# Kernel optimization log

Measured on AMD Instinct MI355X. Metric: run time of the kernel, lower is better.

The kernel has to match this reference:

```python
import jax, jax.numpy as jnp
import numpy as np

N, C_IN, C_OUT, T, V, K = 32, 64, 128, 300, 25, 3
EPS = 1e-5


def setup_inputs() -> dict:
    key = jax.random.key(0)
    ks = jax.random.split(key, 10)
    x = jax.random.normal(ks[0], (N, C_IN, T, V), dtype=jnp.float32)
    # fixed adjacency buffer (requires_grad=False in torch) and learned attention mask
    A = jax.random.uniform(ks[1], (K, V, V), dtype=jnp.float32)
    graph_attn = jnp.ones((K, V, V), dtype=jnp.float32)  # nn.init.constant_(1)
    # per-subset 1x1 conv weights/biases, stacked: [K, C_out, C_in]
    Wg = jax.random.normal(ks[2], (K, C_OUT, C_IN), dtype=jnp.float32) * np.sqrt(2.0 / (C_OUT * K))
    bg = jnp.zeros((K, C_OUT), dtype=jnp.float32)
    # main BN affine (torch init: weight=1e-6, bias=0; use small random for a nontrivial test)
    bn_gamma = jax.random.normal(ks[3], (C_OUT,), dtype=jnp.float32) * 0.1 + 1.0
    bn_beta = jax.random.normal(ks[4], (C_OUT,), dtype=jnp.float32) * 0.1
    # residual branch (in != out): 1x1 conv + BN
    Wr = jax.random.normal(ks[5], (C_OUT, C_IN), dtype=jnp.float32) * np.sqrt(2.0 / C_IN)
    br = jnp.zeros((C_OUT,), dtype=jnp.float32)
    rbn_gamma = jax.random.normal(ks[6], (C_OUT,), dtype=jnp.float32) * 0.1 + 1.0
    rbn_beta = jax.random.normal(ks[7], (C_OUT,), dtype=jnp.float32) * 0.1
    return {"x": x, "A": A, "graph_attn": graph_attn, "Wg": Wg, "bg": bg,
            "bn_gamma": bn_gamma, "bn_beta": bn_beta,
            "Wr": Wr, "br": br, "rbn_gamma": rbn_gamma, "rbn_beta": rbn_beta}


def _batchnorm(z, gamma, beta):
    # training-mode BatchNorm2d: biased batch stats over (N, T, V)
    mean = jnp.mean(z, axis=(0, 2, 3), keepdims=True)
    var = jnp.var(z, axis=(0, 2, 3), keepdims=True)
    zhat = (z - mean) * jax.lax.rsqrt(var + EPS)
    return zhat * gamma[None, :, None, None] + beta[None, :, None, None]


def reference(x, A, graph_attn, Wg, bg, bn_gamma, bn_beta, Wr, br, rbn_gamma, rbn_beta):
    Ae = A * graph_attn                                   # [K, V, V]
    # per-subset graph aggregation: (x.view(N, C*T, V) @ Ae[k])  -> [K, N, C, T, V]
    xA = jnp.einsum('nctv,kvw->knctw', x, Ae)
    # per-subset 1x1 conv then sum over subsets; biases sum as well
    hidden = jnp.einsum('knctv,koc->notv', xA, Wg) + jnp.sum(bg, axis=0)[None, :, None, None]
    hidden = _batchnorm(hidden, bn_gamma, bn_beta)
    # residual: 1x1 conv + BN (since in_channels != out_channels)
    res = jnp.einsum('nctv,oc->notv', x, Wr) + br[None, :, None, None]
    res = _batchnorm(res, rbn_gamma, rbn_beta)
    return hidden + res
```

## Files before the change

### kernel.cpp

```cpp
#include <hip/hip_runtime.h>

typedef __attribute__((ext_vector_type(8))) _Float16 half8;
typedef __attribute__((ext_vector_type(4))) _Float16 half4v;
typedef __attribute__((ext_vector_type(4))) float float4v;
typedef float float4u __attribute__((ext_vector_type(4), aligned(4)));
typedef unsigned long long u64;
typedef unsigned int u32;

#define NB   32
#define CIN  64
#define COUT 128
#define TT   300
#define VV   25
#define EPS  1e-5f
#define M_TOT 240000.0f
#define NBLK 1600
#define NTILE 4800

#define WS_WF    0
#define WS_AEF   65536
#define WS_ST    73728
#define WS_CF    75776
#define WS_WF2   77312
#define WS_HR    1048576
#define WS_PARTP (WS_HR + 137625600)
#define WS_NEED  (WS_PARTP + 3276800)

__device__ __forceinline__ void bar_lds() {
    __builtin_amdgcn_sched_barrier(0);
    asm volatile("s_waitcnt lgkmcnt(0)" ::: "memory");
    __builtin_amdgcn_s_barrier();
    __builtin_amdgcn_sched_barrier(0);
}

__device__ __forceinline__ unsigned short f2h(float f) {
    return __builtin_bit_cast(unsigned short, (_Float16)f);
}
__device__ __forceinline__ float4v mfma16(half8 a, half8 b, float4v c) {
    return __builtin_amdgcn_mfma_f32_16x16x32_f16(a, b, c, 0, 0, 0);
}
__device__ __forceinline__ u32 pk2(float a, float b) {
    return __builtin_bit_cast(u32, __builtin_amdgcn_cvt_pkrtz(a, b));
}
__device__ __forceinline__ int hr_off(int cm, int on) {
    return (cm & 1) ? (2048 + (cm >> 1) * 768 + on * 384)
                    : ((cm >> 1) * 1024 + on * 512);
}

__global__ void prep_kernel(const float* __restrict__ A, const float* __restrict__ ga,
                            const float* __restrict__ Wg, const float* __restrict__ Wr,
                            char* __restrict__ wsb) {
    unsigned short* wf = (unsigned short*)(wsb + WS_WF);
    unsigned short* ae = (unsigned short*)(wsb + WS_AEF);
    float* st = (float*)(wsb + WS_ST);
    int i = blockIdx.x * blockDim.x + threadIdx.x;
    for (; i < 32768 + 4096 + 512; i += gridDim.x * blockDim.x) {
        if (i < 32768) {
            int on = i >> 12, kt = (i >> 9) & 7, l = (i >> 3) & 63, j = i & 7;
            int o = on * 16 + (l & 15);
            int kc = kt * 32 + ((l >> 4) << 3) + j;
            float v = (kc < 192) ? Wg[((kc >> 6) * COUT + o) * CIN + (kc & 63)]
                                 : Wr[o * CIN + (kc - 192)];
            wf[i] = f2h(v);
        } else if (i < 32768 + 4096) {
            int q = i - 32768;
            int k = q >> 10, nt = (q >> 9) & 1, l = (q >> 3) & 63, j = q & 7;
            int v = ((l >> 4) << 3) + j, w = nt * 16 + (l & 15);
            float val = 0.0f;
            if (v < VV && w < VV)
                val = (k < 3) ? A[(k * VV + v) * VV + w] * ga[(k * VV + v) * VV + w]
                              : (v == w ? 1.0f : 0.0f);
            ae[q] = f2h(val);
        } else {
            st[i - 36864] = 0.0f;
        }
    }
}

__global__ __launch_bounds__(256) void red_kernel(const float* __restrict__ part,
                                                  char* __restrict__ wsb) {
    float* st = (float*)(wsb + WS_ST);
    __shared__ float red[4][4];
    const int tid = threadIdx.x, wv = tid >> 6, lane = tid & 63;
    const int i0 = blockIdx.x * 4;
    const int bi = tid >> 2, ii = tid & 3;
    float s = 0.0f;
    for (int b = bi; b < NBLK; b += 64)
        s += part[(size_t)b * 512 + i0 + ii];
    s += __shfl_xor(s, 4);
    s += __shfl_xor(s, 8);
    s += __shfl_xor(s, 16);
    s += __shfl_xor(s, 32);
    if (lane < 4) red[wv][lane] = s;
    __syncthreads();
    if (tid < 4) st[i0 + tid] = red[0][tid] + red[1][tid] + red[2][tid] + red[3][tid];
}

__global__ __launch_bounds__(256) void scale_kernel(
        const float* __restrict__ Wg, const float* __restrict__ Wr,
        const float* __restrict__ g1, const float* __restrict__ b1,
        const float* __restrict__ g2, const float* __restrict__ b2,
        char* __restrict__ wsb, int fillw2) {
    const float* st = (const float*)(wsb + WS_ST);
    float* cf = (float*)(wsb + WS_CF);
    unsigned short* wf2 = (unsigned short*)(wsb + WS_WF2);
    __shared__ float cl[384];
    int tid = threadIdx.x;
    if (tid < 128) {
        int o = tid;
        const float inv_m = 1.0f / M_TOT;
        float mH = st[o] * inv_m,        vH = st[128 + o] * inv_m - mH * mH;
        float mR = st[256 + o] * inv_m,  vR = st[384 + o] * inv_m - mR * mR;
        float scH = g1[o] * rsqrtf(vH + EPS);
        float scR = g2[o] * rsqrtf(vR + EPS);
        float bC  = b1[o] + b2[o] - scH * mH - scR * mR;
        cl[o] = scH; cl[128 + o] = scR; cl[256 + o] = bC;
        if (blockIdx.x == 0) { cf[o] = scH; cf[128 + o] = scR; cf[256 + o] = bC; }
    }
    __syncthreads();
    if (!fillw2) return;
    for (int i = blockIdx.x * 256 + tid; i < 32768; i += gridDim.x * 256) {
        int on = i >> 12, kt = (i >> 9) & 7, l = (i >> 3) & 63, j = i & 7;
        int o = on * 16 + (l & 15);
        int kc = kt * 32 + ((l >> 4) << 3) + j;
        float v = (kc < 192) ? Wg[((kc >> 6) * COUT + o) * CIN + (kc & 63)] * cl[o]
                             : Wr[o * CIN + (kc - 192)] * cl[128 + o];
        wf2[i] = f2h(v);
    }
}

template <int MODE>
__global__ __launch_bounds__(256, 2) void gcn_kernel(
        const float* __restrict__ x, char* __restrict__ wsb, float* __restrict__ out,
        float* __restrict__ part) {
    __shared__ __align__(16) _Float16 xa[64 * 256];
    __shared__ __align__(16) _Float16 xs[2][64][32];
    char* xab = (char*)xa;

    const unsigned short* wf = (const unsigned short*)(wsb + (MODE == 1 ? WS_WF2 : WS_WF));
    const unsigned short* ae = (const unsigned short*)(wsb + WS_AEF);
    const float* cf = (const float*)(wsb + WS_CF);

    const int tid = threadIdx.x, wv = tid >> 6, l = tid & 63;
    const int l15 = l & 15, lq = l >> 4;

    half8 af[2][8];
#pragma unroll
    for (int on = 0; on < 2; ++on)
#pragma unroll
        for (int kt = 0; kt < 8; ++kt)
            af[on][kt] = *(const half8*)&wf[(((wv * 2 + on) * 8 + kt) * 64 + l) * 8];

    half8 aef[4][2];
#pragma unroll
    for (int k = 0; k < 4; ++k)
#pragma unroll
        for (int nt = 0; nt < 2; ++nt)
            aef[k][nt] = *(const half8*)&ae[((k * 2 + nt) * 64 + l) * 8];

    float bC2[2];
    if (MODE == 1) {
#pragma unroll
        for (int on = 0; on < 2; ++on)
            bC2[on] = cf[256 + wv * 32 + on * 16 + l15];
    }

    float sH[2], sH2[2], sR[2], sR2[2];
    if (MODE != 1) {
#pragma unroll
        for (int on = 0; on < 2; ++on) { sH[on] = 0; sH2[on] = 0; sR[on] = 0; sR2[on] = 0; }
    }

    for (int e = tid; e < 896; e += 256) {
        int t = e / 448, r = e % 448;
        xs[t][r / 7][25 + r % 7] = (_Float16)0.0f;
    }

    float4v pre[4];
    auto issue_pre = [&](int n_, int t0_) {
#pragma unroll
        for (int p = 0; p < 4; ++p) {
            int idx = tid + p * 256;
            int c = idx >> 4, i = idx & 15;
            int f0 = i * 4; f0 = f0 > 46 ? 46 : f0;
            const float* g = x + n_ * 480000 + c * 7500 + t0_ * 25 + f0;
            float4u v = *(const float4u*)g;
            pre[p][0] = v[0]; pre[p][1] = v[1]; pre[p][2] = v[2]; pre[p][3] = v[3];
        }
    };
    auto write_xs = [&]() {
#pragma unroll
        for (int p = 0; p < 4; ++p) {
            int idx = tid + p * 256;
            int c = idx >> 4, i = idx & 15;
            int f0 = i * 4; f0 = f0 > 46 ? 46 : f0;
#pragma unroll
            for (int s = 0; s < 4; ++s) {
                int f = f0 + s;
                int tsel = (f >= 25) ? 1 : 0;
                xs[tsel][c][f - tsel * 25] = (_Float16)pre[p][s];
            }
        }
    };

    const int tile0 = blockIdx.x * 3;
    { int n0 = tile0 / 150, t00 = (tile0 % 150) * 2; issue_pre(n0, t00); }
    write_xs();

    for (int it = 0; it < 3; ++it) {
        const int tile = tile0 + it;
        const int n = tile / 150, t0 = (tile % 150) * 2;
        bar_lds();

        const bool hn = (it < 2);
        if (hn) { int tl = tile + 1; issue_pre(tl / 150, (tl % 150) * 2); }

#pragma unroll
        for (int t = 0; t < 2; ++t) {
            half8 xf = *(const half8*)&xs[t][wv * 16 + l15][lq * 8];
#pragma unroll
            for (int k = 0; k < 4; ++k)
#pragma unroll
                for (int nt = 0; nt < 2; ++nt) {
                    float4v c4 = {0.0f, 0.0f, 0.0f, 0.0f};
                    c4 = mfma16(xf, aef[k][nt], c4);
                    int col = t * 32 + nt * 16 + l15;
                    int kcb = (k * 64 + wv * 16 + lq * 4) * 2;
                    u64 pk = ((u64)pk2(c4[2], c4[3]) << 32) | pk2(c4[0], c4[1]);
                    *(u64*)(xab + ((col << 9) + (kcb ^ ((col & 7) << 4)))) = pk;
                }
        }
        bar_lds();

        char* hrw = wsb + WS_HR + (size_t)tile * 28672 + wv * 7168;

        float4v acc[4][2];
        if (MODE != 1) {
#pragma unroll
            for (int cm = 0; cm < 4; ++cm)
#pragma unroll
                for (int on = 0; on < 2; ++on) acc[cm][on] = {0.0f, 0.0f, 0.0f, 0.0f};
#pragma unroll
            for (int kt = 0; kt < 6; ++kt)
#pragma unroll
                for (int cm = 0; cm < 4; ++cm) {
                    int col = cm * 16 + l15;
                    half8 bf = *(const half8*)(xab + ((col << 9) +
                                   ((kt * 64 + lq * 16) ^ ((col & 7) << 4))));
                    acc[cm][0] = mfma16(bf, af[0][kt], acc[cm][0]);
                    acc[cm][1] = mfma16(bf, af[1][kt], acc[cm][1]);
                }
#pragma unroll
            for (int cm = 0; cm < 4; ++cm)
#pragma unroll
                for (int on = 0; on < 2; ++on) {
#pragma unroll
                    for (int r = 0; r < 4; ++r) {
                        float h = acc[cm][on][r];
                        sH[on] += h; sH2[on] += h * h;
                    }
                    if (MODE == 2) {
                        u64 p = (u64)pk2(acc[cm][on][0], acc[cm][on][1]) |
                                ((u64)pk2(acc[cm][on][2], acc[cm][on][3]) << 32);
                        if (!(cm & 1)) {
                            *(u64*)(hrw + hr_off(cm, on) + l * 8) = p;
                        } else if (lq < 3) {
                            *(u64*)(hrw + hr_off(cm, on) + l * 8) = p;
                        }
                    }
                    acc[cm][on] = {0.0f, 0.0f, 0.0f, 0.0f};
                }
#pragma unroll
            for (int kt = 6; kt < 8; ++kt)
#pragma unroll
                for (int cm = 0; cm < 4; ++cm) {
                    int col = cm * 16 + l15;
                    half8 bf = *(const half8*)(xab + ((col << 9) +
                                   ((kt * 64 + lq * 16) ^ ((col & 7) << 4))));
                    acc[cm][0] = mfma16(bf, af[0][kt], acc[cm][0]);
                    acc[cm][1] = mfma16(bf, af[1][kt], acc[cm][1]);
                }
#pragma unroll
            for (int cm = 0; cm < 4; ++cm)
#pragma unroll
                for (int on = 0; on < 2; ++on) {
#pragma unroll
                    for (int r = 0; r < 4; ++r) {
                        float rv = acc[cm][on][r];
                        sR[on] += rv; sR2[on] += rv * rv;
                    }
                    if (MODE == 2) {
                        u64 p = (u64)pk2(acc[cm][on][0], acc[cm][on][1]) |
                                ((u64)pk2(acc[cm][on][2], acc[cm][on][3]) << 32);
                        if (!(cm & 1)) {
                            *(u64*)(hrw + 3584 + hr_off(cm, on) + l * 8) = p;
                        } else if (lq < 3) {
                            *(u64*)(hrw + 3584 + hr_off(cm, on) + l * 8) = p;
                        }
                    }
                }
        } else {
#pragma unroll
            for (int cm = 0; cm < 4; ++cm)
#pragma unroll
                for (int on = 0; on < 2; ++on)
#pragma unroll
                    for (int r = 0; r < 4; ++r) acc[cm][on][r] = bC2[on];
#pragma unroll
            for (int kt = 0; kt < 8; ++kt)
#pragma unroll
                for (int cm = 0; cm < 4; ++cm) {
                    int col = cm * 16 + l15;
                    half8 bf = *(const half8*)(xab + ((col << 9) +
                                   ((kt * 64 + lq * 16) ^ ((col & 7) << 4))));
                    acc[cm][0] = mfma16(bf, af[0][kt], acc[cm][0]);
                    acc[cm][1] = mfma16(bf, af[1][kt], acc[cm][1]);
                }
#pragma unroll
            for (int cm = 0; cm < 4; ++cm) {
                int t = t0 + (cm >> 1);
#pragma unroll
                for (int on = 0; on < 2; ++on) {
                    int o = wv * 32 + on * 16 + l15;
                    float* op = out + ((size_t)(n * COUT + o) * TT + t) * VV;
                    if (!(cm & 1)) {
                        *(float4u*)(op + lq * 4) = acc[cm][on];
                    } else if (lq < 2) {
                        *(float4u*)(op + 16 + lq * 4) = acc[cm][on];
                    } else if (lq == 2) {
                        op[24] = acc[cm][on][0];
                    }
                }
            }
        }

        if (hn) write_xs();

        if (it < 2) {
            __builtin_amdgcn_sched_barrier(0);
            if (MODE == 2) asm volatile("s_waitcnt vmcnt(16) lgkmcnt(0)" ::: "memory");
            else           asm volatile("s_waitcnt vmcnt(0) lgkmcnt(0)" ::: "memory");
            __builtin_amdgcn_s_barrier();
            __builtin_amdgcn_sched_barrier(0);
        }
    }

    if (MODE != 1) {
#pragma unroll
        for (int on = 0; on < 2; ++on) {
            sH[on]  += __shfl_xor(sH[on], 16);  sH[on]  += __shfl_xor(sH[on], 32);
            sH2[on] += __shfl_xor(sH2[on], 16); sH2[on] += __shfl_xor(sH2[on], 32);
            sR[on]  += __shfl_xor(sR[on], 16);  sR[on]  += __shfl_xor(sR[on], 32);
            sR2[on] += __shfl_xor(sR2[on], 16); sR2[on] += __shfl_xor(sR2[on], 32);
        }
        if (l < 16) {
            float* pb = part + (size_t)blockIdx.x * 512;
#pragma unroll
            for (int on = 0; on < 2; ++on) {
                int o = wv * 32 + on * 16 + l15;
                pb[o]       = sH[on];
                pb[128 + o] = sH2[on];
                pb[256 + o] = sR[on];
                pb[384 + o] = sR2[on];
            }
        }
    }
}

__global__ __launch_bounds__(256) void bn_apply(const char* __restrict__ wsb,
                                                float* __restrict__ out) {
    __shared__ u64 lds[3584];
    const float* cf = (const float*)(wsb + WS_CF);
    const int tile = blockIdx.x;
    const int n = tile / 150, t0 = (tile % 150) * 2;
    const int tid = threadIdx.x;

    const u64* src = (const u64*)(wsb + WS_HR + (size_t)tile * 28672);
#pragma unroll
    for (int i = 0; i < 14; ++i) lds[tid + i * 256] = src[tid + i * 256];
    __syncthreads();

#pragma unroll
    for (int i = 0; i < 7; ++i) {
        int j2 = tid + i * 256;
        int row = j2 / 7, q = j2 - row * 7;
        int o = row >> 1, t = row & 1;
        int v0 = (q < 6) ? q * 4 : 24;
        int cm = t * 2 + (v0 >> 4);
        int lq = (v0 & 15) >> 2;
        int ll = lq * 16 + (o & 15);
        int wv = o >> 5, on = (o >> 4) & 1;
        int offq = (cm & 1) ? (256 + (cm >> 1) * 96 + on * 48)
                            : ((cm >> 1) * 128 + on * 64);
        u64 h64 = lds[wv * 896 + offq + ll];
        u64 r64 = lds[wv * 896 + 448 + offq + ll];
        half4v h4 = __builtin_bit_cast(half4v, h64);
        half4v r4 = __builtin_bit_cast(half4v, r64);
        float scH = cf[o], scR = cf[128 + o], bC = cf[256 + o];
        float* op = out + ((size_t)(n * COUT + o) * TT + t0 + t) * VV + v0;
        if (q < 6) {
            float4u v;
#pragma unroll
            for (int k = 0; k < 4; ++k)
                v[k] = scH * (float)h4[k] + scR * (float)r4[k] + bC;
            *(float4u*)op = v;
        } else {
            op[0] = scH * (float)h4[0] + scR * (float)r4[0] + bC;
        }
    }
}

extern "C" void kernel_launch(void* const* d_in, const int* in_sizes, int n_in,
                              void* d_out, int out_size, void* d_ws, size_t ws_size,
                              hipStream_t stream) {
    const float* x        = (const float*)d_in[0];
    const float* A        = (const float*)d_in[1];
    const float* ga       = (const float*)d_in[2];
    const float* Wg       = (const float*)d_in[3];
    const float* bn_gamma = (const float*)d_in[5];
    const float* bn_beta  = (const float*)d_in[6];
    const float* Wr       = (const float*)d_in[7];
    const float* rbn_g    = (const float*)d_in[9];
    const float* rbn_b    = (const float*)d_in[10];
    char* wsb  = (char*)d_ws;
    float* out = (float*)d_out;

    const bool primary = ws_size >= (size_t)WS_NEED + 4096;
    float* partP = (float*)(wsb + WS_PARTP);
    float* partF = (float*)(wsb + WS_HR);

    prep_kernel<<<64, 256, 0, stream>>>(A, ga, Wg, Wr, wsb);
    if (primary) {
        gcn_kernel<2><<<NBLK, 256, 0, stream>>>(x, wsb, nullptr, partP);
        red_kernel<<<128, 256, 0, stream>>>(partP, wsb);
        scale_kernel<<<64, 256, 0, stream>>>(Wg, Wr, bn_gamma, bn_beta, rbn_g, rbn_b, wsb, 0);
        bn_apply<<<NTILE, 256, 0, stream>>>(wsb, out);
    } else {
        gcn_kernel<0><<<NBLK, 256, 0, stream>>>(x, wsb, nullptr, partF);
        red_kernel<<<128, 256, 0, stream>>>(partF, wsb);
        scale_kernel<<<64, 256, 0, stream>>>(Wg, Wr, bn_gamma, bn_beta, rbn_g, rbn_b, wsb, 1);
        gcn_kernel<1><<<NBLK, 256, 0, stream>>>(x, wsb, out, partF);
    }
}
```

Baseline: 120.4 us.

## Launch one block per tile instead of three pipelined tiles per block

The gcn kernel now processes a single tile per block and launches 4800 blocks instead of 1600 blocks that each looped over three tiles with software-prefetched x loads. The partial-statistics buffer and reduction grow to one entry per tile. This trades the intra-block prefetch pipelining for more blocks and occupancy-based latency hiding. In exchange it repeats the per-block weight and adjacency register loads three times as often and makes red_kernel read three times more partials.

```diff
diff --git a/kernel.cpp b/kernel.cpp
--- a/kernel.cpp
+++ b/kernel.cpp
@@ -14,7 +14,6 @@
 #define VV   25
 #define EPS  1e-5f
 #define M_TOT 240000.0f
-#define NBLK 1600
 #define NTILE 4800
 
 #define WS_WF    0
@@ -24,7 +23,7 @@
 #define WS_WF2   77312
 #define WS_HR    1048576
 #define WS_PARTP (WS_HR + 137625600)
-#define WS_NEED  (WS_PARTP + 3276800)
+#define WS_NEED  (WS_PARTP + 9830400)
 
 __device__ __forceinline__ void bar_lds() {
     __builtin_amdgcn_sched_barrier(0);
@@ -85,7 +84,7 @@
     const int i0 = blockIdx.x * 4;
     const int bi = tid >> 2, ii = tid & 3;
     float s = 0.0f;
-    for (int b = bi; b < NBLK; b += 64)
+    for (int b = bi; b < NTILE; b += 64)
         s += part[(size_t)b * 512 + i0 + ii];
     s += __shfl_xor(s, 4);
     s += __shfl_xor(s, 8);
@@ -144,6 +143,20 @@
     const int tid = threadIdx.x, wv = tid >> 6, l = tid & 63;
     const int l15 = l & 15, lq = l >> 4;
 
+    const int tile = blockIdx.x;
+    const int n = tile / 150, t0 = (tile % 150) * 2;
+
+    float4v pre[4];
+#pragma unroll
+    for (int p = 0; p < 4; ++p) {
+        int idx = tid + p * 256;
+        int c = idx >> 4, i = idx & 15;
+        int f0 = i * 4; f0 = f0 > 46 ? 46 : f0;
+        const float* g = x + n * 480000 + c * 7500 + t0 * 25 + f0;
+        float4u v = *(const float4u*)g;
+        pre[p][0] = v[0]; pre[p][1] = v[1]; pre[p][2] = v[2]; pre[p][3] = v[3];
+    }
+
     half8 af[2][8];
 #pragma unroll
     for (int on = 0; on < 2; ++on)
@@ -163,189 +176,114 @@
 #pragma unroll
         for (int on = 0; on < 2; ++on)
             bC2[on] = cf[256 + wv * 32 + on * 16 + l15];
-    }
-
-    float sH[2], sH2[2], sR[2], sR2[2];
-    if (MODE != 1) {
-#pragma unroll
-        for (int on = 0; on < 2; ++on) { sH[on] = 0; sH2[on] = 0; sR[on] = 0; sR2[on] = 0; }
     }
 
     for (int e = tid; e < 896; e += 256) {
         int t = e / 448, r = e % 448;
         xs[t][r / 7][25 + r % 7] = (_Float16)0.0f;
     }
-
-    float4v pre[4];
-    auto issue_pre = [&](int n_, int t0_) {
-#pragma unroll
-        for (int p = 0; p < 4; ++p) {
-            int idx = tid + p * 256;
-            int c = idx >> 4, i = idx & 15;
-            int f0 = i * 4; f0 = f0 > 46 ? 46 : f0;
-            const float* g = x + n_ * 480000 + c * 7500 + t0_ * 25 + f0;
-            float4u v = *(const float4u*)g;
-            pre[p][0] = v[0]; pre[p][1] = v[1]; pre[p][2] = v[2]; pre[p][3] = v[3];
-        }
-    };
-    auto write_xs = [&]() {
-#pragma unroll
-        for (int p = 0; p < 4; ++p) {
-            int idx = tid + p * 256;
-            int c = idx >> 4, i = idx & 15;
-            int f0 = i * 4; f0 = f0 > 46 ? 46 : f0;
-#pragma unroll
-            for (int s = 0; s < 4; ++s) {
-                int f = f0 + s;
-                int tsel = (f >= 25) ? 1 : 0;
-                xs[tsel][c][f - tsel * 25] = (_Float16)pre[p][s];
-            }
-        }
-    };
-
-    const int tile0 = blockIdx.x * 3;
-    { int n0 = tile0 / 150, t00 = (tile0 % 150) * 2; issue_pre(n0, t00); }
-    write_xs();
-
-    for (int it = 0; it < 3; ++it) {
-        const int tile = tile0 + it;
-        const int n = tile / 150, t0 = (tile % 150) * 2;
-        bar_lds();
-
-        const bool hn = (it < 2);
-        if (hn) { int tl = tile + 1; issue_pre(tl / 150, (tl % 150) * 2); }
-
-#pragma unroll
-        for (int t = 0; t < 2; ++t) {
-            half8 xf = *(const half8*)&xs[t][wv * 16 + l15][lq * 8];
-#pragma unroll
-            for (int k = 0; k < 4; ++k)
-#pragma unroll
-                for (int nt = 0; nt < 2; ++nt) {
-                    float4v c4 = {0.0f, 0.0f, 0.0f, 0.0f};
-                    c4 = mfma16(xf, aef[k][nt], c4);
-                    int col = t * 32 + nt * 16 + l15;
-                    int kcb = (k * 64 + wv * 16 + lq * 4) * 2;
-                    u64 pk = ((u64)pk2(c4[2], c4[3]) << 32) | pk2(c4[0], c4[1]);
-                    *(u64*)(xab + ((col << 9) + (kcb ^ ((col & 7) << 4)))) = pk;
+#pragma unroll
+    for (int p = 0; p < 4; ++p) {
+        int idx = tid + p * 256;
+        int c = idx >> 4, i = idx & 15;
+        int f0 = i * 4; f0 = f0 > 46 ? 46 : f0;
+#pragma unroll
+        for (int s = 0; s < 4; ++s) {
+            int f = f0 + s;
+            int tsel = (f >= 25) ? 1 : 0;
+            xs[tsel][c][f - tsel * 25] = (_Float16)pre[p][s];
+        }
+    }
+    bar_lds();
+
+#pragma unroll
+    for (int t = 0; t < 2; ++t) {
+        half8 xf = *(const half8*)&xs[t][wv * 16 + l15][lq * 8];
+#pragma unroll
+        for (int k = 0; k < 4; ++k)
+#pragma unroll
+            for (int nt = 0; nt < 2; ++nt) {
+                float4v c4 = {0.0f, 0.0f, 0.0f, 0.0f};
+                c4 = mfma16(xf, aef[k][nt], c4);
+                int col = t * 32 + nt * 16 + l15;
+                int kcb = (k * 64 + wv * 16 + lq * 4) * 2;
+                u64 pk = ((u64)pk2(c4[2], c4[3]) << 32) | pk2(c4[0], c4[1]);
+                *(u64*)(xab + ((col << 9) + (kcb ^ ((col & 7) << 4)))) = pk;
+            }
+    }
+    bar_lds();
+
+    char* hrw = wsb + WS_HR + (size_t)tile * 28672 + wv * 7168;
+
+    float sH[2], sH2[2], sR[2], sR2[2];
+#pragma unroll
+    for (int on = 0; on < 2; ++on) { sH[on] = 0; sH2[on] = 0; sR[on] = 0; sR2[on] = 0; }
+
+    float4v acc[4][2];
+    if (MODE != 1) {
+#pragma unroll
+        for (int cm = 0; cm < 4; ++cm)
+#pragma unroll
+            for (int on = 0; on < 2; ++on) acc[cm][on] = {0.0f, 0.0f, 0.0f, 0.0f};
+#pragma unroll
+        for (int kt = 0; kt < 6; ++kt)
+#pragma unroll
+            for (int cm = 0; cm < 4; ++cm) {
+                int col = cm * 16 + l15;
+                half8 bf = *(const half8*)(xab + ((col << 9) +
+                               ((kt * 64 + lq * 16) ^ ((col & 7) << 4))));
+                acc[cm][0] = mfma16(bf, af[0][kt], acc[cm][0]);
+                acc[cm][1] = mfma16(bf, af[1][kt], acc[cm][1]);
+            }
+#pragma unroll
+        for (int cm = 0; cm < 4; ++cm)
+#pragma unroll
+            for (int on = 0; on < 2; ++on) {
+#pragma unroll
+                for (int r = 0; r < 4; ++r) {
+                    float h = acc[cm][on][r];
+                    sH[on] += h; sH2[on] += h * h;
                 }
-        }
-        bar_lds();
-
-        char* hrw = wsb + WS_HR + (size_t)tile * 28672 + wv * 7168;
-
-        float4v acc[4][2];
-        if (MODE != 1) {
-#pragma unroll
-            for (int cm = 0; cm < 4; ++cm)
-#pragma unroll
-                for (int on = 0; on < 2; ++on) acc[cm][on] = {0.0f, 0.0f, 0.0f, 0.0f};
-#pragma unroll
-            for (int kt = 0; kt < 6; ++kt)
-#pragma unroll
-                for (int cm = 0; cm < 4; ++cm) {
-                    int col = cm * 16 + l15;
-                    half8 bf = *(const half8*)(xab + ((col << 9) +
-                                   ((kt * 64 + lq * 16) ^ ((col & 7) << 4))));
-                    acc[cm][0] = mfma16(bf, af[0][kt], acc[cm][0]);
-                    acc[cm][1] = mfma16(bf, af[1][kt], acc[cm][1]);
-                }
-#pragma unroll
-            for (int cm = 0; cm < 4; ++cm)
-#pragma unroll
-                for (int on = 0; on < 2; ++on) {
-#pragma unroll
-                    for (int r = 0; r < 4; ++r) {
-                        float h = acc[cm][on][r];
-                        sH[on] += h; sH2[on] += h * h;
-                    }
-                    if (MODE == 2) {
-                        u64 p = (u64)pk2(acc[cm][on][0], acc[cm][on][1]) |
-                                ((u64)pk2(acc[cm][on][2], acc[cm][on][3]) << 32);
-                        if (!(cm & 1)) {
-                            *(u64*)(hrw + hr_off(cm, on) + l * 8) = p;
-                        } else if (lq < 3) {
-                            *(u64*)(hrw + hr_off(cm, on) + l * 8) = p;
-                        }
-                    }
-                    acc[cm][on] = {0.0f, 0.0f, 0.0f, 0.0f};
-                }
-#pragma unroll
-            for (int kt = 6; kt < 8; ++kt)
-#pragma unroll
-                for (int cm = 0; cm < 4; ++cm) {
-                    int col = cm * 16 + l15;
-                    half8 bf = *(const half8*)(xab + ((col << 9) +
-                                   ((kt * 64 + lq * 16) ^ ((col & 7) << 4))));
-                    acc[cm][0] = mfma16(bf, af[0][kt], acc[cm][0]);
-                    acc[cm][1] = mfma16(bf, af[1][kt], acc[cm][1]);
-                }
-#pragma unroll
-            for (int cm = 0; cm < 4; ++cm)
-#pragma unroll
-                for (int on = 0; on < 2; ++on) {
-#pragma unroll
-                    for (int r = 0; r < 4; ++r) {
-                        float rv = acc[cm][on][r];
-                        sR[on] += rv; sR2[on] += rv * rv;
-                    }
-                    if (MODE == 2) {
-                        u64 p = (u64)pk2(acc[cm][on][0], acc[cm][on][1]) |
-                                ((u64)pk2(acc[cm][on][2], acc[cm][on][3]) << 32);
-                        if (!(cm & 1)) {
-                            *(u64*)(hrw + 3584 + hr_off(cm, on) + l * 8) = p;
-                        } else if (lq < 3) {
-                            *(u64*)(hrw + 3584 + hr_off(cm, on) + l * 8) = p;
-                        }
+                if (MODE == 2) {
+                    u64 p = (u64)pk2(acc[cm][on][0], acc[cm][on][1]) |
+                            ((u64)pk2(acc[cm][on][2], acc[cm][on][3]) << 32);
+                    if (!(cm & 1)) {
+                        *(u64*)(hrw + hr_off(cm, on) + l * 8) = p;
+                    } else if (lq < 3) {
+                        *(u64*)(hrw + hr_off(cm, on) + l * 8) = p;
                     }
                 }
-        } else {
-#pragma unroll
-            for (int cm = 0; cm < 4; ++cm)
-#pragma unroll
-                for (int on = 0; on < 2; ++on)
-#pragma unroll
-                    for (int r = 0; r < 4; ++r) acc[cm][on][r] = bC2[on];
-#pragma unroll
-            for (int kt = 0; kt < 8; ++kt)
-#pragma unroll
-                for (int cm = 0; cm < 4; ++cm) {
-                    int col = cm * 16 + l15;
-                    half8 bf = *(const half8*)(xab + ((col << 9) +
-                                   ((kt * 64 + lq * 16) ^ ((col & 7) << 4))));
-                    acc[cm][0] = mfma16(bf, af[0][kt], acc[cm][0]);
-                    acc[cm][1] = mfma16(bf, af[1][kt], acc[cm][1]);
+                acc[cm][on] = {0.0f, 0.0f, 0.0f, 0.0f};
+            }
+#pragma unroll
+        for (int kt = 6; kt < 8; ++kt)
+#pragma unroll
+            for (int cm = 0; cm < 4; ++cm) {
+                int col = cm * 16 + l15;
+                half8 bf = *(const half8*)(xab + ((col << 9) +
+                               ((kt * 64 + lq * 16) ^ ((col & 7) << 4))));
+                acc[cm][0] = mfma16(bf, af[0][kt], acc[cm][0]);
+                acc[cm][1] = mfma16(bf, af[1][kt], acc[cm][1]);
+            }
+#pragma unroll
+        for (int cm = 0; cm < 4; ++cm)
+#pragma unroll
+            for (int on = 0; on < 2; ++on) {
+#pragma unroll
+                for (int r = 0; r < 4; ++r) {
+                    float rv = acc[cm][on][r];
+                    sR[on] += rv; sR2[on] += rv * rv;
                 }
-#pragma unroll
-            for (int cm = 0; cm < 4; ++cm) {
-                int t = t0 + (cm >> 1);
-#pragma unroll
-                for (int on = 0; on < 2; ++on) {
-                    int o = wv * 32 + on * 16 + l15;
-                    float* op = out + ((size_t)(n * COUT + o) * TT + t) * VV;
+                if (MODE == 2) {
+                    u64 p = (u64)pk2(acc[cm][on][0], acc[cm][on][1]) |
+                            ((u64)pk2(acc[cm][on][2], acc[cm][on][3]) << 32);
                     if (!(cm & 1)) {
-                        *(float4u*)(op + lq * 4) = acc[cm][on];
-                    } else if (lq < 2) {
-                        *(float4u*)(op + 16 + lq * 4) = acc[cm][on];
-                    } else if (lq == 2) {
-                        op[24] = acc[cm][on][0];
+                        *(u64*)(hrw + 3584 + hr_off(cm, on) + l * 8) = p;
+                    } else if (lq < 3) {
+                        *(u64*)(hrw + 3584 + hr_off(cm, on) + l * 8) = p;
                     }
                 }
             }
-        }
-
-        if (hn) write_xs();
-
-        if (it < 2) {
-            __builtin_amdgcn_sched_barrier(0);
-            if (MODE == 2) asm volatile("s_waitcnt vmcnt(16) lgkmcnt(0)" ::: "memory");
-            else           asm volatile("s_waitcnt vmcnt(0) lgkmcnt(0)" ::: "memory");
-            __builtin_amdgcn_s_barrier();
-            __builtin_amdgcn_sched_barrier(0);
-        }
-    }
-
-    if (MODE != 1) {
 #pragma unroll
         for (int on = 0; on < 2; ++on) {
             sH[on]  += __shfl_xor(sH[on], 16);  sH[on]  += __shfl_xor(sH[on], 32);
@@ -354,7 +292,7 @@
             sR2[on] += __shfl_xor(sR2[on], 16); sR2[on] += __shfl_xor(sR2[on], 32);
         }
         if (l < 16) {
-            float* pb = part + (size_t)blockIdx.x * 512;
+            float* pb = part + (size_t)tile * 512;
 #pragma unroll
             for (int on = 0; on < 2; ++on) {
                 int o = wv * 32 + on * 16 + l15;
@@ -362,6 +300,39 @@
                 pb[128 + o] = sH2[on];
                 pb[256 + o] = sR[on];
                 pb[384 + o] = sR2[on];
+            }
+        }
+    } else {
+#pragma unroll
+        for (int cm = 0; cm < 4; ++cm)
+#pragma unroll
+            for (int on = 0; on < 2; ++on)
+#pragma unroll
+                for (int r = 0; r < 4; ++r) acc[cm][on][r] = bC2[on];
+#pragma unroll
+        for (int kt = 0; kt < 8; ++kt)
+#pragma unroll
+            for (int cm = 0; cm < 4; ++cm) {
+                int col = cm * 16 + l15;
+                half8 bf = *(const half8*)(xab + ((col << 9) +
+                               ((kt * 64 + lq * 16) ^ ((col & 7) << 4))));
+                acc[cm][0] = mfma16(bf, af[0][kt], acc[cm][0]);
+                acc[cm][1] = mfma16(bf, af[1][kt], acc[cm][1]);
+            }
+#pragma unroll
+        for (int cm = 0; cm < 4; ++cm) {
+            int t = t0 + (cm >> 1);
+#pragma unroll
+            for (int on = 0; on < 2; ++on) {
+                int o = wv * 32 + on * 16 + l15;
+                float* op = out + ((size_t)(n * COUT + o) * TT + t) * VV;
+                if (!(cm & 1)) {
+                    *(float4u*)(op + lq * 4) = acc[cm][on];
+                } else if (lq < 2) {
+                    *(float4u*)(op + 16 + lq * 4) = acc[cm][on];
+                } else if (lq == 2) {
+                    op[24] = acc[cm][on][0];
+                }
             }
         }
     }
@@ -431,14 +402,14 @@
 
     prep_kernel<<<64, 256, 0, stream>>>(A, ga, Wg, Wr, wsb);
     if (primary) {
-        gcn_kernel<2><<<NBLK, 256, 0, stream>>>(x, wsb, nullptr, partP);
+        gcn_kernel<2><<<NTILE, 256, 0, stream>>>(x, wsb, nullptr, partP);
         red_kernel<<<128, 256, 0, stream>>>(partP, wsb);
         scale_kernel<<<64, 256, 0, stream>>>(Wg, Wr, bn_gamma, bn_beta, rbn_g, rbn_b, wsb, 0);
         bn_apply<<<NTILE, 256, 0, stream>>>(wsb, out);
     } else {
-        gcn_kernel<0><<<NBLK, 256, 0, stream>>>(x, wsb, nullptr, partF);
+        gcn_kernel<0><<<NTILE, 256, 0, stream>>>(x, wsb, nullptr, partF);
         red_kernel<<<128, 256, 0, stream>>>(partF, wsb);
         scale_kernel<<<64, 256, 0, stream>>>(Wg, Wr, bn_gamma, bn_beta, rbn_g, rbn_b, wsb, 1);
-        gcn_kernel<1><<<NBLK, 256, 0, stream>>>(x, wsb, out, partF);
-    }
-}
+        gcn_kernel<1><<<NTILE, 256, 0, stream>>>(x, wsb, out, partF);
+    }
+}
```

Result: slower. 147.8 us (+22.8%).
